# Optimization experiments

Hardware: AMD Instinct MI355X
Metric: run time of the kernel (lower is better)

Reference implementation:

```python
import jax, jax.numpy as jnp
import numpy as np

NEGATIVE = 5
MORPH_VOCAB = 200002  # morph_size + 2 (pad + extra row)
D = 128
B = 32768
M = 6


def setup_inputs() -> dict:
    key = jax.random.key(0)
    k = jax.random.split(key, 7)
    data = jax.random.randint(k[0], (B, 2 + 2 * NEGATIVE), 0, 2, dtype=jnp.int64 if jax.config.jax_enable_x64 else jnp.int32)
    word2morph = jax.random.randint(k[1], (B, M), 0, 200000)
    word2morph_mask = jax.random.uniform(k[2], (B, M, 1), dtype=jnp.float32)
    ctx2morph = jax.random.randint(k[3], (B, 1 + NEGATIVE, M), 0, 200000)
    ctx2morph_mask = jax.random.uniform(k[4], (B, 1 + NEGATIVE, M, 1), dtype=jnp.float32)
    # learned tables; torch inits emb0 ~ U(-0.5/D, 0.5/D) and emb1 = 0;
    # use small random values so the reference exercises nontrivial math
    emb0 = jax.random.uniform(k[5], (MORPH_VOCAB, D), minval=-0.5 / D, maxval=0.5 / D, dtype=jnp.float32)
    emb1 = jax.random.uniform(k[6], (MORPH_VOCAB, D), minval=-0.5 / D, maxval=0.5 / D, dtype=jnp.float32)
    return {
        "data": data,
        "word2morph": word2morph,
        "word2morph_mask": word2morph_mask,
        "ctx2morph": ctx2morph,
        "ctx2morph_mask": ctx2morph_mask,
        "emb0": emb0,
        "emb1": emb1,
    }


def reference(data, word2morph, word2morph_mask, ctx2morph, ctx2morph_mask, emb0, emb1):
    neg_mask = data[:, 2 + NEGATIVE:].astype(jnp.float32)              # [B, neg]
    # masked embedding-bag sums over morphemes
    w_embs = jnp.sum(emb0[word2morph] * word2morph_mask, axis=1)        # [B, D]
    c_embs = jnp.sum(emb1[ctx2morph[:, 0]] * ctx2morph_mask[:, 0], axis=1)  # [B, D]
    n_embs = jnp.sum(emb1[ctx2morph[:, 1:1 + NEGATIVE]] * ctx2morph_mask[:, 1:1 + NEGATIVE], axis=2)  # [B, neg, D]
    # dot-product scores
    pos_ips = jnp.sum(w_embs * c_embs, axis=1)                          # [B]
    neg_ips = jnp.einsum("bnd,bd->bn", n_embs, w_embs)                 # [B, neg]
    # clamped logsigmoid losses
    pos_loss = jnp.sum(-jax.nn.log_sigmoid(jnp.clip(pos_ips, -10.0, 10.0)))
    neg_loss = jnp.sum(-jax.nn.log_sigmoid(jnp.clip(-neg_ips, -10.0, 10.0)) * neg_mask)
    return pos_loss + neg_loss
```

## Files before the change

### kernel.cpp

```cpp
#include <hip/hip_runtime.h>

#define NEG 5
#define MM 6
#define NCTX 6
#define NC 36
#define DD 128
#define WPB 4
#define RPW 2
#define RPB (WPB * RPW)
#define DROW 12
#define S_SCALE 4096.0f
#define INV_S (1.0f / 4096.0f)

typedef float v2f __attribute__((ext_vector_type(2)));
typedef float v4f __attribute__((ext_vector_type(4)));

__device__ __forceinline__ int geti(const int4& v, int c) {
    switch (c) { case 0: return v.x; case 1: return v.y; case 2: return v.z; default: return v.w; }
}
__device__ __forceinline__ float getf(const float4& v, int c) {
    switch (c) { case 0: return v.x; case 1: return v.y; case 2: return v.z; default: return v.w; }
}

__global__ __launch_bounds__(256) void sg_w_kernel(
    const int*   __restrict__ w2m,
    const float* __restrict__ w2m_mask,
    const float* __restrict__ emb0,
    float*       __restrict__ wbuf,
    int B)
{
    const int lane  = threadIdx.x & 63;
    const int wid   = threadIdx.x >> 6;
    const int sub   = lane >> 5;
    const int slane = lane & 31;
    const int base  = lane & 32;
    const int b     = blockIdx.x * RPB + wid * RPW + sub;
    if (b >= B) return;

    int wi = 0; float wmk = 0.f;
    if (slane < MM)           wi  = w2m[(size_t)b * MM + slane];
    else if (slane < 2 * MM)  wmk = w2m_mask[(size_t)b * MM + (slane - MM)];

    const unsigned long long e0p = (unsigned long long)emb0;
    const unsigned int doff = (unsigned int)slane << 4;

    v4f rr[MM]; float mk[MM];
    #pragma unroll
    for (int m = 0; m < MM; ++m) {
        const int idx = __shfl(wi, base + m, 64);
        mk[m]         = __shfl(wmk, base + MM + m, 64);
        const unsigned int voff = ((unsigned int)idx << 9) + doff;
        asm volatile("global_load_dwordx4 %0, %1, %2"
                     : "=v"(rr[m]) : "v"(voff), "s"(e0p) : "memory");
    }
    asm volatile("s_waitcnt vmcnt(0)" ::: "memory");
    __builtin_amdgcn_sched_barrier(0);

    v4f acc = {0.f, 0.f, 0.f, 0.f};
    #pragma unroll
    for (int m = 0; m < MM; ++m) {
        acc[0] += rr[m][0] * mk[m]; acc[1] += rr[m][1] * mk[m];
        acc[2] += rr[m][2] * mk[m]; acc[3] += rr[m][3] * mk[m];
    }
    *reinterpret_cast<v4f*>(wbuf + (size_t)b * DD + slane * 4) = acc;
}

__global__ __launch_bounds__(256) void cvt_fp8_kernel(
    const float* __restrict__ emb1, unsigned int* __restrict__ q, long n4)
{
    const long stride = (long)gridDim.x * 256;
    for (long i = (long)blockIdx.x * 256 + threadIdx.x; i < n4; i += stride) {
        v4f v = __builtin_nontemporal_load(reinterpret_cast<const v4f*>(emb1) + i);
        int r = 0;
        r = __builtin_amdgcn_cvt_pk_fp8_f32(v[0] * S_SCALE, v[1] * S_SCALE, r, false);
        r = __builtin_amdgcn_cvt_pk_fp8_f32(v[2] * S_SCALE, v[3] * S_SCALE, r, true);
        q[i] = (unsigned int)r;
    }
}

__global__ __launch_bounds__(256) void sg_dot8_kernel(
    const int*   __restrict__ data,
    const int*   __restrict__ c2m,
    const float* __restrict__ c2m_mask,
    const unsigned int* __restrict__ q,
    const float* __restrict__ wbuf,
    float*       __restrict__ out,
    int B)
{
    const int lane  = threadIdx.x & 63;
    const int wid   = threadIdx.x >> 6;
    const int sub   = lane >> 5;
    const int slane = lane & 31;
    const int base  = lane & 32;
    const int b     = blockIdx.x * RPB + wid * RPW + sub;

    float loss = 0.0f;
    if (b < B) {
        int4 ci = {0,0,0,0}; float4 cmk = {0.f,0.f,0.f,0.f};
        int nm = 0;
        if (slane < 9)       ci  = reinterpret_cast<const int4*>(c2m + (size_t)b * NC)[slane];
        else if (slane < 18) cmk = reinterpret_cast<const float4*>(c2m_mask + (size_t)b * NC)[slane - 9];
        if (slane < NEG)     nm  = data[(size_t)b * DROW + 2 + NEG + slane];

        float nmf[NEG];
        #pragma unroll
        for (int n = 0; n < NEG; ++n) nmf[n] = (float)__shfl(nm, base + n, 64);

        const int d0 = slane * 4;
        float4 w = *reinterpret_cast<const float4*>(wbuf + (size_t)b * DD + d0);
        w.x *= INV_S; w.y *= INV_S; w.z *= INV_S; w.w *= INV_S;

        const unsigned long long qp = (unsigned long long)q;
        const unsigned int soff = (unsigned int)slane << 2;
        unsigned int rq[NC];
        #pragma unroll
        for (int t = 0; t < NC; ++t) {
            const int k = t >> 2, c = t & 3;
            const int idx = __shfl(geti(ci, c), base + k, 64);
            const unsigned int voff = ((unsigned int)idx << 7) + soff;
            asm volatile("global_load_dword %0, %1, %2"
                         : "=v"(rq[t]) : "v"(voff), "s"(qp) : "memory");
        }
        asm volatile("s_waitcnt vmcnt(0)" ::: "memory");
        __builtin_amdgcn_sched_barrier(0);

        float p[NCTX];
        #pragma unroll
        for (int j = 0; j < NCTX; ++j) {
            float pj = 0.f;
            #pragma unroll
            for (int m = 0; m < MM; ++m) {
                const int t = j * MM + m;
                const int k = t >> 2, c = t & 3;
                const float mk = __shfl(getf(cmk, c), base + 9 + k, 64);
                v2f lo = __builtin_amdgcn_cvt_pk_f32_fp8(rq[t], false);
                v2f hi = __builtin_amdgcn_cvt_pk_f32_fp8(rq[t], true);
                pj += mk * (lo[0] * w.x + lo[1] * w.y + hi[0] * w.z + hi[1] * w.w);
            }
            p[j] = pj;
        }

        #pragma unroll
        for (int j = 0; j < NCTX; ++j) {
            float v = p[j];
            #pragma unroll
            for (int off = 16; off >= 1; off >>= 1) v += __shfl_xor(v, off, 64);
            p[j] = v;
        }
        if (slane == 0) {
            float x = fminf(fmaxf(p[0], -10.0f), 10.0f);
            loss = log1pf(expf(-x));
            #pragma unroll
            for (int n = 0; n < NEG; ++n) {
                float y = fminf(fmaxf(-p[1 + n], -10.0f), 10.0f);
                loss += log1pf(expf(-y)) * nmf[n];
            }
        }
    }
    __shared__ float sacc[RPB];
    if (slane == 0) sacc[wid * RPW + sub] = loss;
    __syncthreads();
    if (threadIdx.x == 0) {
        float s = 0.0f;
        #pragma unroll
        for (int i = 0; i < RPB; ++i) s += sacc[i];
        atomicAdd(out, s);
    }
}

__global__ __launch_bounds__(256) void sg_fused8_kernel(
    const int*   __restrict__ data,
    const int*   __restrict__ w2m,
    const float* __restrict__ w2m_mask,
    const int*   __restrict__ c2m,
    const float* __restrict__ c2m_mask,
    const float* __restrict__ emb0,
    const unsigned int* __restrict__ q,
    float*       __restrict__ out,
    int B)
{
    const int lane  = threadIdx.x & 63;
    const int wid   = threadIdx.x >> 6;
    const int sub   = lane >> 5;
    const int slane = lane & 31;
    const int base  = lane & 32;
    const int b     = blockIdx.x * RPB + wid * RPW + sub;

    float loss = 0.0f;
    if (b < B) {
        int4 ci = {0,0,0,0}; float4 cmk = {0.f,0.f,0.f,0.f};
        int wi = 0; float wmk = 0.f; int nm = 0;
        if (slane < 9)       ci  = reinterpret_cast<const int4*>(c2m + (size_t)b * NC)[slane];
        else if (slane < 18) cmk = reinterpret_cast<const float4*>(c2m_mask + (size_t)b * NC)[slane - 9];
        else if (slane < 24) wi  = w2m[(size_t)b * MM + (slane - 18)];
        else if (slane < 30) wmk = w2m_mask[(size_t)b * MM + (slane - 24)];
        if (slane < NEG) nm = data[(size_t)b * DROW + 2 + NEG + slane];

        float nmf[NEG];
        #pragma unroll
        for (int n = 0; n < NEG; ++n) nmf[n] = (float)__shfl(nm, base + n, 64);

        const int d0 = slane * 4;
        float4 wr[MM]; float wmks[MM];
        #pragma unroll
        for (int m = 0; m < MM; ++m) {
            const int idx = __shfl(wi, base + 18 + m, 64);
            wmks[m] = __shfl(wmk, base + 24 + m, 64);
            wr[m] = *reinterpret_cast<const float4*>(emb0 + (size_t)idx * DD + d0);
        }
        unsigned int rq[NC];
        #pragma unroll
        for (int t = 0; t < NC; ++t) {
            const int k = t >> 2, c = t & 3;
            const int idx = __shfl(geti(ci, c), base + k, 64);
            rq[t] = q[(size_t)idx * 32 + slane];
        }

        float4 w = {0.f,0.f,0.f,0.f};
        #pragma unroll
        for (int m = 0; m < MM; ++m) {
            w.x += wr[m].x * wmks[m]; w.y += wr[m].y * wmks[m];
            w.z += wr[m].z * wmks[m]; w.w += wr[m].w * wmks[m];
        }
        w.x *= INV_S; w.y *= INV_S; w.z *= INV_S; w.w *= INV_S;

        float p[NCTX];
        #pragma unroll
        for (int j = 0; j < NCTX; ++j) {
            float pj = 0.f;
            #pragma unroll
            for (int m = 0; m < MM; ++m) {
                const int t = j * MM + m;
                const int k = t >> 2, c = t & 3;
                const float mk = __shfl(getf(cmk, c), base + 9 + k, 64);
                v2f lo = __builtin_amdgcn_cvt_pk_f32_fp8(rq[t], false);
                v2f hi = __builtin_amdgcn_cvt_pk_f32_fp8(rq[t], true);
                pj += mk * (lo[0] * w.x + lo[1] * w.y + hi[0] * w.z + hi[1] * w.w);
            }
            p[j] = pj;
        }

        #pragma unroll
        for (int j = 0; j < NCTX; ++j) {
            float v = p[j];
            #pragma unroll
            for (int off = 16; off >= 1; off >>= 1) v += __shfl_xor(v, off, 64);
            p[j] = v;
        }
        if (slane == 0) {
            float x = fminf(fmaxf(p[0], -10.0f), 10.0f);
            loss = log1pf(expf(-x));
            #pragma unroll
            for (int n = 0; n < NEG; ++n) {
                float y = fminf(fmaxf(-p[1 + n], -10.0f), 10.0f);
                loss += log1pf(expf(-y)) * nmf[n];
            }
        }
    }
    __shared__ float sacc[RPB];
    if (slane == 0) sacc[wid * RPW + sub] = loss;
    __syncthreads();
    if (threadIdx.x == 0) {
        float s = 0.0f;
        #pragma unroll
        for (int i = 0; i < RPB; ++i) s += sacc[i];
        atomicAdd(out, s);
    }
}

extern "C" void kernel_launch(void* const* d_in, const int* in_sizes, int n_in,
                              void* d_out, int out_size, void* d_ws, size_t ws_size,
                              hipStream_t stream) {
    const int*   data     = (const int*)  d_in[0];
    const int*   w2m      = (const int*)  d_in[1];
    const float* w2m_mask = (const float*)d_in[2];
    const int*   c2m      = (const int*)  d_in[3];
    const float* c2m_mask = (const float*)d_in[4];
    const float* emb0     = (const float*)d_in[5];
    const float* emb1     = (const float*)d_in[6];
    float* out = (float*)d_out;

    const int B     = in_sizes[1] / MM;
    const int vocab = in_sizes[6] / DD;
    const int blocks = (B + RPB - 1) / RPB;

    (void)hipMemsetAsync(out, 0, sizeof(float), stream);

    const size_t qbytes = (size_t)vocab * DD;
    const size_t wbytes = (size_t)B * DD * sizeof(float);
    const long   n4     = (long)vocab * 32;

    if (ws_size >= qbytes + wbytes) {
        unsigned int* q = (unsigned int*)d_ws;
        float* wbuf = (float*)((char*)d_ws + qbytes);
        sg_w_kernel<<<blocks, 64 * WPB, 0, stream>>>(w2m, w2m_mask, emb0, wbuf, B);
        cvt_fp8_kernel<<<2048, 256, 0, stream>>>(emb1, q, n4);
        sg_dot8_kernel<<<blocks, 64 * WPB, 0, stream>>>(data, c2m, c2m_mask, q, wbuf, out, B);
    } else if (ws_size >= qbytes) {
        unsigned int* q = (unsigned int*)d_ws;
        cvt_fp8_kernel<<<2048, 256, 0, stream>>>(emb1, q, n4);
        sg_fused8_kernel<<<blocks, 64 * WPB, 0, stream>>>(
            data, w2m, w2m_mask, c2m, c2m_mask, emb0, q, out, B);
    }
}
```

Baseline: 117.0 us.

## Map one row per full wavefront in fp8 dot kernel with scalar index loads

```diff
diff --git a/kernel.cpp b/kernel.cpp
--- a/kernel.cpp
+++ b/kernel.cpp
@@ -78,7 +78,7 @@
     }
 }
 
-__global__ __launch_bounds__(256) void sg_dot8_kernel(
+__global__ __launch_bounds__(256) void sg_dot8s_kernel(
     const int*   __restrict__ data,
     const int*   __restrict__ c2m,
     const float* __restrict__ c2m_mask,
@@ -87,42 +87,19 @@
     float*       __restrict__ out,
     int B)
 {
-    const int lane  = threadIdx.x & 63;
-    const int wid   = threadIdx.x >> 6;
-    const int sub   = lane >> 5;
-    const int slane = lane & 31;
-    const int base  = lane & 32;
-    const int b     = blockIdx.x * RPB + wid * RPW + sub;
+    const int lane = threadIdx.x & 63;
+    const int wid  = __builtin_amdgcn_readfirstlane(threadIdx.x >> 6);
+    const int b    = blockIdx.x * WPB + wid;
 
     float loss = 0.0f;
     if (b < B) {
-        int4 ci = {0,0,0,0}; float4 cmk = {0.f,0.f,0.f,0.f};
-        int nm = 0;
-        if (slane < 9)       ci  = reinterpret_cast<const int4*>(c2m + (size_t)b * NC)[slane];
-        else if (slane < 18) cmk = reinterpret_cast<const float4*>(c2m_mask + (size_t)b * NC)[slane - 9];
-        if (slane < NEG)     nm  = data[(size_t)b * DROW + 2 + NEG + slane];
-
-        float nmf[NEG];
-        #pragma unroll
-        for (int n = 0; n < NEG; ++n) nmf[n] = (float)__shfl(nm, base + n, 64);
-
-        const int d0 = slane * 4;
-        float4 w = *reinterpret_cast<const float4*>(wbuf + (size_t)b * DD + d0);
-        w.x *= INV_S; w.y *= INV_S; w.z *= INV_S; w.w *= INV_S;
-
-        const unsigned long long qp = (unsigned long long)q;
-        const unsigned int soff = (unsigned int)slane << 2;
-        unsigned int rq[NC];
-        #pragma unroll
-        for (int t = 0; t < NC; ++t) {
-            const int k = t >> 2, c = t & 3;
-            const int idx = __shfl(geti(ci, c), base + k, 64);
-            const unsigned int voff = ((unsigned int)idx << 7) + soff;
-            asm volatile("global_load_dword %0, %1, %2"
-                         : "=v"(rq[t]) : "v"(voff), "s"(qp) : "memory");
-        }
-        asm volatile("s_waitcnt vmcnt(0)" ::: "memory");
-        __builtin_amdgcn_sched_barrier(0);
+        const int*   cp = c2m      + (size_t)b * NC;
+        const float* mp = c2m_mask + (size_t)b * NC;
+
+        v2f w = *reinterpret_cast<const v2f*>(wbuf + (size_t)b * DD + lane * 2);
+        w[0] *= INV_S; w[1] *= INV_S;
+
+        const char* qb = (const char*)q + (unsigned int)lane * 2;
 
         float p[NCTX];
         #pragma unroll
@@ -131,11 +108,12 @@
             #pragma unroll
             for (int m = 0; m < MM; ++m) {
                 const int t = j * MM + m;
-                const int k = t >> 2, c = t & 3;
-                const float mk = __shfl(getf(cmk, c), base + 9 + k, 64);
-                v2f lo = __builtin_amdgcn_cvt_pk_f32_fp8(rq[t], false);
-                v2f hi = __builtin_amdgcn_cvt_pk_f32_fp8(rq[t], true);
-                pj += mk * (lo[0] * w.x + lo[1] * w.y + hi[0] * w.z + hi[1] * w.w);
+                const int   idx = cp[t];
+                const float mk  = mp[t];
+                const unsigned int u =
+                    *reinterpret_cast<const unsigned short*>(qb + ((size_t)idx << 7));
+                v2f lo = __builtin_amdgcn_cvt_pk_f32_fp8(u, false);
+                pj += mk * (lo[0] * w[0] + lo[1] * w[1]);
             }
             p[j] = pj;
         }
@@ -144,26 +122,30 @@
         for (int j = 0; j < NCTX; ++j) {
             float v = p[j];
             #pragma unroll
-            for (int off = 16; off >= 1; off >>= 1) v += __shfl_xor(v, off, 64);
+            for (int off = 32; off >= 1; off >>= 1)
+                v += __shfl_xor(v, off, 64);
             p[j] = v;
         }
-        if (slane == 0) {
+
+        if (lane == 0) {
             float x = fminf(fmaxf(p[0], -10.0f), 10.0f);
             loss = log1pf(expf(-x));
             #pragma unroll
             for (int n = 0; n < NEG; ++n) {
                 float y = fminf(fmaxf(-p[1 + n], -10.0f), 10.0f);
-                loss += log1pf(expf(-y)) * nmf[n];
-            }
-        }
-    }
-    __shared__ float sacc[RPB];
-    if (slane == 0) sacc[wid * RPW + sub] = loss;
+                float msk = (float)data[(size_t)b * DROW + 2 + NEG + n];
+                loss += log1pf(expf(-y)) * msk;
+            }
+        }
+    }
+
+    __shared__ float sacc[WPB];
+    if (lane == 0) sacc[wid] = loss;
     __syncthreads();
     if (threadIdx.x == 0) {
         float s = 0.0f;
         #pragma unroll
-        for (int i = 0; i < RPB; ++i) s += sacc[i];
+        for (int i = 0; i < WPB; ++i) s += sacc[i];
         atomicAdd(out, s);
     }
 }
@@ -295,7 +277,8 @@
         float* wbuf = (float*)((char*)d_ws + qbytes);
         sg_w_kernel<<<blocks, 64 * WPB, 0, stream>>>(w2m, w2m_mask, emb0, wbuf, B);
         cvt_fp8_kernel<<<2048, 256, 0, stream>>>(emb1, q, n4);
-        sg_dot8_kernel<<<blocks, 64 * WPB, 0, stream>>>(data, c2m, c2m_mask, q, wbuf, out, B);
+        sg_dot8s_kernel<<<(B + WPB - 1) / WPB, 64 * WPB, 0, stream>>>(
+            data, c2m, c2m_mask, q, wbuf, out, B);
     } else if (ws_size >= qbytes) {
         unsigned int* q = (unsigned int*)d_ws;
         cvt_fp8_kernel<<<2048, 256, 0, stream>>>(emb1, q, n4);
```

After: 166.5 us. 1.42x slower.
